# Kernel tuning notes

Measured on AMD Instinct MI355X. Metric: run time of the kernel, lower is better.

Reference implementation:

```python
import jax, jax.numpy as jnp
import numpy as np

N = 50000      # nodes
E = 400000     # edges per hop
IN = 256       # in_channels
H = 4          # heads
C = 64         # out_channels per head
NEG = 0.2      # leaky relu negative slope


def setup_inputs() -> dict:
    key = jax.random.key(0)
    ks = jax.random.split(key, 10)
    x = jax.random.normal(ks[0], (N, IN), dtype=jnp.float32)
    edge_index1 = jax.random.randint(ks[1], (2, E), 0, N, dtype=jnp.int32)
    edge_index2 = jax.random.randint(ks[2], (2, E), 0, N, dtype=jnp.int32)
    s = 0.05
    Wl0 = jax.random.normal(ks[3], (IN, H * C), dtype=jnp.float32) * s
    Wr0 = jax.random.normal(ks[4], (IN, H * C), dtype=jnp.float32) * s
    att0 = jax.random.normal(ks[5], (H, C), dtype=jnp.float32) * s
    Wl1 = jax.random.normal(ks[6], (IN, H * C), dtype=jnp.float32) * s
    Wr1 = jax.random.normal(ks[7], (IN, H * C), dtype=jnp.float32) * s
    att1 = jax.random.normal(ks[8], (H, C), dtype=jnp.float32) * s
    return {"x": x, "Wl0": Wl0, "Wr0": Wr0, "att0": att0,
            "Wl1": Wl1, "Wr1": Wr1, "att1": att1,
            "edge_index1": edge_index1, "edge_index2": edge_index2}


def _gatv2_hop(x, Wl, Wr, att, src, dst):
    """One GATv2Conv hop (bias=False, residual=False, eval-mode dropout, concat=False)."""
    n = x.shape[0]
    xl = (x @ Wl).reshape(n, H, C)   # source-side projection
    xr = (x @ Wr).reshape(n, H, C)   # target-side projection
    # edge-wise GATv2 score: a^T leaky_relu(x_l[j] + x_r[i])
    m = jax.nn.leaky_relu(xl[src] + xr[dst], NEG)            # [E, H, C]
    e = jnp.einsum('ehc,hc->eh', m, att)                     # [E, H]
    # segment softmax over incoming edges of each destination node
    e_max = jax.lax.stop_gradient(
        jax.ops.segment_max(e, dst, num_segments=n))         # [N, H]
    ex = jnp.exp(e - e_max[dst])
    denom = jax.ops.segment_sum(ex, dst, num_segments=n)     # [N, H]
    alpha = ex / (denom[dst] + 1e-16)                        # [E, H]
    msg = xl[src] * alpha[:, :, None]                        # [E, H, C]
    out = jax.ops.segment_sum(msg, dst, num_segments=n)      # [N, H, C]
    return out.mean(axis=1)                                  # concat=False -> mean heads


def reference(x, Wl0, Wr0, att0, Wl1, Wr1, att1, edge_index1, edge_index2):
    n = x.shape[0]
    # hop 0: add_self_loops=True
    loop = jnp.arange(n, dtype=edge_index1.dtype)
    src0 = jnp.concatenate([edge_index1[0], loop])
    dst0 = jnp.concatenate([edge_index1[1], loop])
    out = _gatv2_hop(x, Wl0, Wr0, att0, src0, dst0)
    # hop 1: no self loops, scaled by 1/(k+1) = 1/2
    out = out + _gatv2_hop(x, Wl1, Wr1, att1, edge_index2[0], edge_index2[1]) / 2.0
    return out
```

## Files before the change

### kernel.cpp

```cpp
#include <hip/hip_runtime.h>

typedef unsigned int uint;
typedef unsigned short ushort;

typedef __bf16 bf16x8 __attribute__((ext_vector_type(8)));
typedef float f32x4 __attribute__((ext_vector_type(4)));

#define CAP 48
#define RSTR 136

__device__ __forceinline__ float bf2f(ushort u) {
    return __uint_as_float(((uint)u) << 16);
}
__device__ __forceinline__ ushort f2bf(float f) {
    uint u = __float_as_uint(f);
    u += 0x7fffu + ((u >> 16) & 1u);
    return (ushort)(u >> 16);
}
__device__ __forceinline__ void load_lds16(const ushort* g, ushort* l) {
    __builtin_amdgcn_global_load_lds(
        (const __attribute__((address_space(1))) void*)g,
        (__attribute__((address_space(3))) void*)l, 16, 0, 0);
}

template<int CTRL>
__device__ __forceinline__ float dppadd(float p) {
    int t = __builtin_amdgcn_update_dpp(0, __float_as_int(p), CTRL, 0xf, 0xf, true);
    return p + __int_as_float(t);
}

__global__ __launch_bounds__(256) void prep(
    const float* __restrict__ X, ushort* __restrict__ Xb, int Nrows, int Mpad,
    const float* __restrict__ Wl0, const float* __restrict__ Wr0,
    const float* __restrict__ Wl1, const float* __restrict__ Wr1,
    ushort* __restrict__ Wt,
    int* __restrict__ cnt0, int* __restrict__ cnt1)
{
    const int BX = Mpad / 8;
    int blk = blockIdx.x;
    if (blk < BX) {
        int i = blk * 256 + threadIdx.x;
        int base = i * 8;
        int row = base >> 8;
        ushort o[8];
        if (row < Nrows) {
            float4 v0 = *(const float4*)(X + base);
            float4 v1 = *(const float4*)(X + base + 4);
            o[0] = f2bf(v0.x); o[1] = f2bf(v0.y); o[2] = f2bf(v0.z); o[3] = f2bf(v0.w);
            o[4] = f2bf(v1.x); o[5] = f2bf(v1.y); o[6] = f2bf(v1.z); o[7] = f2bf(v1.w);
        } else {
#pragma unroll
            for (int j = 0; j < 8; j++) o[j] = 0;
        }
        *(uint4*)(Xb + base) = *(const uint4*)o;
        return;
    }
    blk -= BX;
    if (blk < 1024) {
        int n = blk;
        int k = threadIdx.x;
        const float* W = (n < 256) ? Wl0 : (n < 512) ? Wr0 : (n < 768) ? Wl1 : Wr1;
        Wt[n * 256 + k] = f2bf(W[k * 256 + (n & 255)]);
        return;
    }
    blk -= 1024;
    int d = blk * 256 + threadIdx.x;
    if (d < Nrows) {
        cnt0[d] = 0;
        cnt1[d] = 0;
    }
}

__global__ __launch_bounds__(256) void csr_scatter2(
    const int* __restrict__ ei1, const int* __restrict__ ei2,
    int* __restrict__ cnt0, int* __restrict__ srcs0,
    int* __restrict__ cnt1, int* __restrict__ srcs1,
    int E1, int E2)
{
    int e = blockIdx.x * 256 + threadIdx.x;
    if (e < E1) {
        int d = ei1[E1 + e];
        int pos = atomicAdd(&cnt0[d], 1);
        if (pos < CAP) srcs0[(size_t)d * CAP + pos] = ei1[e];
    } else if (e < E1 + E2) {
        int e2 = e - E1;
        int d = ei2[E2 + e2];
        int pos = atomicAdd(&cnt1[d], 1);
        if (pos < CAP) srcs1[(size_t)d * CAP + pos] = ei2[e2];
    }
}

__global__ __launch_bounds__(256, 2) void gemm_mfma(
    const ushort* __restrict__ Xb,
    const ushort* __restrict__ Wt,
    ushort* __restrict__ XP,
    int Nrows)
{
    __shared__ ushort SH[2 * 128 * 64];
    ushort* As = SH;
    ushort* Bs = SH + 128 * 64;

    const int tid = threadIdx.x;
    const int w = tid >> 6, l = tid & 63;
    const int wm = w & 1, wn = w >> 1;
    const int m0 = blockIdx.y * 128;
    const int n0g = blockIdx.x * 128;

    f32x4 acc[4][4];
#pragma unroll
    for (int i = 0; i < 4; i++)
#pragma unroll
        for (int j = 0; j < 4; j++) acc[i][j] = (f32x4)(0.f);

    const int fr = l & 15, fq = l >> 4;
    int a_off[2][4], b_off[2][4];
#pragma unroll
    for (int g = 0; g < 2; g++)
#pragma unroll
        for (int t = 0; t < 4; t++) {
            int c = g * 4 + fq;
            int rA = wm * 64 + t * 16 + fr;
            a_off[g][t] = (rA * 8 + ((c + rA) & 7)) * 8;
            int rB = wn * 64 + t * 16 + fr;
            b_off[g][t] = (rB * 8 + ((c + rB) & 7)) * 8;
        }

    for (int k0 = 0; k0 < 256; k0 += 64) {
        __syncthreads();
#pragma unroll
        for (int rnd = 0; rnd < 4; rnd++) {
            int slot = rnd * 256 + tid;
            int row = slot >> 3;
            int c = ((slot & 7) - row) & 7;
            load_lds16(Xb + (size_t)(m0 + row) * 256 + k0 + c * 8,
                       &As[(rnd * 256 + w * 64) * 8]);
            load_lds16(Wt + (size_t)(n0g + row) * 256 + k0 + c * 8,
                       &Bs[(rnd * 256 + w * 64) * 8]);
        }
        __syncthreads();

#pragma unroll
        for (int g = 0; g < 2; g++) {
            bf16x8 a[4], b[4];
#pragma unroll
            for (int t = 0; t < 4; t++) {
                a[t] = *(const bf16x8*)(As + a_off[g][t]);
                b[t] = *(const bf16x8*)(Bs + b_off[g][t]);
            }
#pragma unroll
            for (int mi = 0; mi < 4; mi++)
#pragma unroll
                for (int ni = 0; ni < 4; ni++)
                    acc[mi][ni] = __builtin_amdgcn_mfma_f32_16x16x32_bf16(
                        a[mi], b[ni], acc[mi][ni], 0, 0, 0);
        }
    }

    ushort* OUT = XP + (size_t)(n0g >> 8) * ((size_t)Nrows * 256);
    const int colbase = n0g & 255;
    const int cb = wn * 64 + fr;
#pragma unroll
    for (int r = 0; r < 2; r++) {
        __syncthreads();
#pragma unroll
        for (int mm = 0; mm < 2; mm++) {
            int mi = 2 * r + mm;
            int brb = (wm * 32 + mm * 16 + fq * 4) * RSTR + cb;
#pragma unroll
            for (int reg = 0; reg < 4; reg++)
#pragma unroll
                for (int ni = 0; ni < 4; ni++)
                    SH[brb + reg * RSTR + ni * 16] = f2bf(acc[mi][ni][reg]);
        }
        __syncthreads();
        int br = tid >> 2;
        int grow = m0 + (br >> 5) * 64 + (2 * r + ((br >> 4) & 1)) * 16 + (br & 15);
        bool ok = (grow < Nrows);
        int cc = (tid & 3) * 8;
#pragma unroll
        for (int q = 0; q < 4; q++) {
            uint4 v = *(const uint4*)(SH + br * RSTR + cc + q * 32);
            if (ok) *(uint4*)(OUT + (size_t)grow * 256 + colbase + cc + q * 32) = v;
        }
    }
}

__device__ __forceinline__ uint4 pair_load(const ushort* __restrict__ XL, int sv,
                                           int e, int cp, uint hl, uint sub16)
{
    int eA = (e     < cp) ? e     : cp;
    int eB = (e + 1 < cp) ? e + 1 : cp;
    uint sA = (uint)__builtin_amdgcn_readlane(sv, eA) * 512u;
    uint sB = (uint)__builtin_amdgcn_readlane(sv, eB) * 512u;
    uint off = sA + hl * (sB - sA) + sub16;
    return *(const uint4*)((const char*)XL + off);
}

__device__ __forceinline__ void eaccp(uint4 raw, int deadB, uint hl,
    const float* __restrict__ xr8, const float* __restrict__ av,
    float* __restrict__ acc, float& den)
{
    float x[8];
    x[0] = __uint_as_float(raw.x << 16);
    x[1] = __uint_as_float(raw.x & 0xffff0000u);
    x[2] = __uint_as_float(raw.y << 16);
    x[3] = __uint_as_float(raw.y & 0xffff0000u);
    x[4] = __uint_as_float(raw.z << 16);
    x[5] = __uint_as_float(raw.z & 0xffff0000u);
    x[6] = __uint_as_float(raw.w << 16);
    x[7] = __uint_as_float(raw.w & 0xffff0000u);
    float p0 = 0.f, p1 = 0.f;
#pragma unroll
    for (int j = 0; j < 4; j++) {
        float t = x[j] + xr8[j];
        float lr = fmaxf(t, 0.2f * t);
        p0 = fmaf(av[j], lr, p0);
    }
#pragma unroll
    for (int j = 4; j < 8; j++) {
        float t = x[j] + xr8[j];
        float lr = fmaxf(t, 0.2f * t);
        p1 = fmaf(av[j], lr, p1);
    }
    float p = p0 + p1;
    p = dppadd<0xB1>(p);
    p = dppadd<0x4E>(p);
    p = dppadd<0x141>(p);
    float pe = __expf(p);
    if (deadB & (int)hl) pe = 0.f;
    den += pe;
#pragma unroll
    for (int j = 0; j < 8; j++) acc[j] = fmaf(pe, x[j], acc[j]);
}

__device__ __forceinline__ void gat_hop(
    const ushort* __restrict__ XL, const ushort* __restrict__ XR,
    const float* __restrict__ att, const int* __restrict__ cnt,
    const int* __restrict__ srcs, int self, int d, int lane,
    uint hl, uint sub, uint sub16,
    float* __restrict__ acc, float& den)
{
    uint4 xrr = *(const uint4*)((const char*)XR + (uint)d * 512u + sub16);
    float xr8[8];
    xr8[0] = __uint_as_float(xrr.x << 16);
    xr8[1] = __uint_as_float(xrr.x & 0xffff0000u);
    xr8[2] = __uint_as_float(xrr.y << 16);
    xr8[3] = __uint_as_float(xrr.y & 0xffff0000u);
    xr8[4] = __uint_as_float(xrr.z << 16);
    xr8[5] = __uint_as_float(xrr.z & 0xffff0000u);
    xr8[6] = __uint_as_float(xrr.w << 16);
    xr8[7] = __uint_as_float(xrr.w & 0xffff0000u);
    float av[8];
    *(float4*)(av)     = *(const float4*)(att + sub * 8);
    *(float4*)(av + 4) = *(const float4*)(att + sub * 8 + 4);

#pragma unroll
    for (int j = 0; j < 8; j++) acc[j] = 0.f;
    den = 0.f;

    int m = __builtin_amdgcn_readfirstlane(cnt[d]);
    if (m > CAP) m = CAP;
    const int mt = m + self;
    if (mt <= 0) return;

    int idx = lane - self;
    int mm1 = (m > 0) ? (m - 1) : 0;
    int slot = idx < 0 ? 0 : (idx > mm1 ? mm1 : idx);
    int sv = srcs[(size_t)d * CAP + slot];
    if (self && lane == 0) sv = d;

    const int cp = mt - 1;
    uint4 pf0 = pair_load(XL, sv, 0, cp, hl, sub16);
    uint4 pf1 = pair_load(XL, sv, 2, cp, hl, sub16);
    for (int i = 0; i < mt; i += 4) {
        uint4 c0 = pf0, c1 = pf1;
        pf0 = pair_load(XL, sv, i + 4, cp, hl, sub16);
        pf1 = pair_load(XL, sv, i + 6, cp, hl, sub16);
        eaccp(c0, (i + 1 >= mt) ? 1 : 0, hl, xr8, av, acc, den);
        if (i + 2 < mt)
            eaccp(c1, (i + 3 >= mt) ? 1 : 0, hl, xr8, av, acc, den);
    }
}

__global__ __launch_bounds__(256) void gat_fused(
    const ushort* __restrict__ XL0, const ushort* __restrict__ XR0,
    const float* __restrict__ att0,
    const int* __restrict__ cnt0, const int* __restrict__ srcs0,
    int self0, float scale0,
    const ushort* __restrict__ XL1, const ushort* __restrict__ XR1,
    const float* __restrict__ att1,
    const int* __restrict__ cnt1, const int* __restrict__ srcs1,
    float scale1,
    const float* __restrict__ base, float* __restrict__ outp, int N)
{
    int d = blockIdx.x * 4 + (threadIdx.x >> 6);
    if (d >= N) return;
    int lane = threadIdx.x & 63;
    uint hl = (uint)(lane >> 5);
    uint sub = (uint)(lane & 31);
    uint sub16 = sub * 16u;

    float acc0[8], den0;
    gat_hop(XL0, XR0, att0, cnt0, srcs0, self0, d, lane, hl, sub, sub16, acc0, den0);

    float v[8];
    den0 += __shfl_xor(den0, 32);
    float s0 = scale0 / (den0 + 1e-16f);
    if (cnt1) {
        float acc1[8], den1;
        gat_hop(XL1, XR1, att1, cnt1, srcs1, 0, d, lane, hl, sub, sub16, acc1, den1);
        den1 += __shfl_xor(den1, 32);
        float s1 = scale1 / (den1 + 1e-16f);
#pragma unroll
        for (int j = 0; j < 8; j++) v[j] = acc0[j] * s0 + acc1[j] * s1;
    } else {
#pragma unroll
        for (int j = 0; j < 8; j++) v[j] = acc0[j] * s0;
    }
#pragma unroll
    for (int j = 0; j < 8; j++) {
        v[j] += __shfl_xor(v[j], 8);
        v[j] += __shfl_xor(v[j], 16);
        v[j] += __shfl_xor(v[j], 32);
    }
    if (lane < 8) {
        float* dst = outp + (size_t)d * 64 + lane * 8;
        float4 w0 = {v[0], v[1], v[2], v[3]};
        float4 w1 = {v[4], v[5], v[6], v[7]};
        if (base) {
            float4 b0 = *(const float4*)(base + (size_t)d * 64 + lane * 8);
            float4 b1 = *(const float4*)(base + (size_t)d * 64 + lane * 8 + 4);
            w0.x += b0.x; w0.y += b0.y; w0.z += b0.z; w0.w += b0.w;
            w1.x += b1.x; w1.y += b1.y; w1.z += b1.z; w1.w += b1.w;
        }
        *(float4*)dst = w0;
        *(float4*)(dst + 4) = w1;
    }
}

extern "C" void kernel_launch(void* const* d_in, const int* in_sizes, int n_in,
                              void* d_out, int out_size, void* d_ws, size_t ws_size,
                              hipStream_t stream)
{
    const float* x    = (const float*)d_in[0];
    const float* Wl0  = (const float*)d_in[1];
    const float* Wr0  = (const float*)d_in[2];
    const float* att0 = (const float*)d_in[3];
    const float* Wl1  = (const float*)d_in[4];
    const float* Wr1  = (const float*)d_in[5];
    const float* att1 = (const float*)d_in[6];
    const int* ei1 = (const int*)d_in[7];
    const int* ei2 = (const int*)d_in[8];

    const int N  = in_sizes[0] / 256;
    const int E1 = in_sizes[7] / 2;
    const int E2 = in_sizes[8] / 2;
    const int Mpad = ((N + 127) / 128) * 128;
    const size_t NB = (size_t)N * 256;

    char* ws = (char*)d_ws;
    size_t off = 0;
    ushort* Xb  = (ushort*)(ws + off); off += (size_t)Mpad * 256 * sizeof(ushort);
    ushort* Wt  = (ushort*)(ws + off); off += (size_t)1024 * 256 * sizeof(ushort);
    int* cnt0   = (int*)(ws + off);    off += (size_t)N * sizeof(int);
    int* cnt1   = (int*)(ws + off);    off += (size_t)N * sizeof(int);
    int* srcs0  = (int*)(ws + off);    off += (size_t)N * CAP * sizeof(int);
    int* srcs1  = (int*)(ws + off);    off += (size_t)N * CAP * sizeof(int);
    ushort* XP  = (ushort*)(ws + off);
    size_t need_mega = off + 4 * NB * sizeof(ushort);
    const bool mega = (ws_size >= need_mega);
    float* outf = (float*)d_out;

    const int BX = Mpad / 8;
    int prep_blocks = BX + 1024 + (N + 255) / 256;
    prep<<<prep_blocks, 256, 0, stream>>>(x, Xb, N, Mpad, Wl0, Wr0, Wl1, Wr1,
                                          Wt, cnt0, cnt1);
    const int SB = (E1 + E2 + 255) / 256;
    csr_scatter2<<<SB, 256, 0, stream>>>(
        ei1, ei2, cnt0, srcs0, cnt1, srcs1, E1, E2);

    int aggblk = (N + 3) / 4;
    if (mega) {
        gemm_mfma<<<dim3(8, Mpad / 128), 256, 0, stream>>>(Xb, Wt, XP, N);
        gat_fused<<<aggblk, 256, 0, stream>>>(
            XP, XP + NB, att0, cnt0, srcs0, 1, 0.25f,
            XP + 2 * NB, XP + 3 * NB, att1, cnt1, srcs1, 0.125f,
            nullptr, outf, N);
    } else {
        gemm_mfma<<<dim3(4, Mpad / 128), 256, 0, stream>>>(Xb, Wt, XP, N);
        gat_fused<<<aggblk, 256, 0, stream>>>(
            XP, XP + NB, att0, cnt0, srcs0, 1, 0.25f,
            nullptr, nullptr, nullptr, nullptr, nullptr, 0.f,
            nullptr, outf, N);
        gemm_mfma<<<dim3(4, Mpad / 128), 256, 0, stream>>>(Xb, Wt + 512 * 256, XP, N);
        gat_fused<<<aggblk, 256, 0, stream>>>(
            XP, XP + NB, att1, cnt1, srcs1, 0, 0.125f,
            nullptr, nullptr, nullptr, nullptr, nullptr, 0.f,
            outf, outf, N);
    }
}
```

Baseline: 270.9 us.

## Merge CSR scatter into GEMM launch and pack aggregation math as float2

The edge scatter kernel is folded into the GEMM launch as extra blocks in a 1D grid, so the atomic CSR build runs alongside the MFMA tiles instead of as its own serialized launch. Counter zeroing moves from the prep kernel to a hipMemsetAsync. The edge accumulation math is rewritten on float2 vectors so the compiler can emit packed FP32 ops (v_pk_fma/v_pk_mul) on MI355X. This removes one launch and idle time between kernels, but the GEMM blocks, which use 2-per-CU occupancy, now share the machine with atomic-heavy scatter blocks.

```diff
diff --git a/kernel.cpp b/kernel.cpp
--- a/kernel.cpp
+++ b/kernel.cpp
@@ -5,6 +5,7 @@
 
 typedef __bf16 bf16x8 __attribute__((ext_vector_type(8)));
 typedef float f32x4 __attribute__((ext_vector_type(4)));
+typedef float f32x2 __attribute__((ext_vector_type(2)));
 
 #define CAP 48
 #define RSTR 136
@@ -22,6 +23,12 @@
         (const __attribute__((address_space(1))) void*)g,
         (__attribute__((address_space(3))) void*)l, 16, 0, 0);
 }
+__device__ __forceinline__ f32x2 up2(uint u) {
+    f32x2 r;
+    r.x = __uint_as_float(u << 16);
+    r.y = __uint_as_float(u & 0xffff0000u);
+    return r;
+}
 
 template<int CTRL>
 __device__ __forceinline__ float dppadd(float p) {
@@ -33,8 +40,7 @@
     const float* __restrict__ X, ushort* __restrict__ Xb, int Nrows, int Mpad,
     const float* __restrict__ Wl0, const float* __restrict__ Wr0,
     const float* __restrict__ Wl1, const float* __restrict__ Wr1,
-    ushort* __restrict__ Wt,
-    int* __restrict__ cnt0, int* __restrict__ cnt1)
+    ushort* __restrict__ Wt)
 {
     const int BX = Mpad / 8;
     int blk = blockIdx.x;
@@ -56,46 +62,38 @@
         return;
     }
     blk -= BX;
-    if (blk < 1024) {
-        int n = blk;
-        int k = threadIdx.x;
-        const float* W = (n < 256) ? Wl0 : (n < 512) ? Wr0 : (n < 768) ? Wl1 : Wr1;
-        Wt[n * 256 + k] = f2bf(W[k * 256 + (n & 255)]);
-        return;
-    }
-    blk -= 1024;
-    int d = blk * 256 + threadIdx.x;
-    if (d < Nrows) {
-        cnt0[d] = 0;
-        cnt1[d] = 0;
-    }
-}
-
-__global__ __launch_bounds__(256) void csr_scatter2(
+    int n = blk;
+    int k = threadIdx.x;
+    const float* W = (n < 256) ? Wl0 : (n < 512) ? Wr0 : (n < 768) ? Wl1 : Wr1;
+    Wt[n * 256 + k] = f2bf(W[k * 256 + (n & 255)]);
+}
+
+__global__ __launch_bounds__(256, 2) void gemm_scatter(
+    const ushort* __restrict__ Xb,
+    const ushort* __restrict__ Wt,
+    ushort* __restrict__ XP,
+    int Nrows, int GB, int cshift,
     const int* __restrict__ ei1, const int* __restrict__ ei2,
     int* __restrict__ cnt0, int* __restrict__ srcs0,
     int* __restrict__ cnt1, int* __restrict__ srcs1,
     int E1, int E2)
 {
-    int e = blockIdx.x * 256 + threadIdx.x;
-    if (e < E1) {
-        int d = ei1[E1 + e];
-        int pos = atomicAdd(&cnt0[d], 1);
-        if (pos < CAP) srcs0[(size_t)d * CAP + pos] = ei1[e];
-    } else if (e < E1 + E2) {
-        int e2 = e - E1;
-        int d = ei2[E2 + e2];
-        int pos = atomicAdd(&cnt1[d], 1);
-        if (pos < CAP) srcs1[(size_t)d * CAP + pos] = ei2[e2];
-    }
-}
-
-__global__ __launch_bounds__(256, 2) void gemm_mfma(
-    const ushort* __restrict__ Xb,
-    const ushort* __restrict__ Wt,
-    ushort* __restrict__ XP,
-    int Nrows)
-{
+    int blk = blockIdx.x;
+    if (blk >= GB) {
+        int e = (blk - GB) * 256 + threadIdx.x;
+        if (e < E1) {
+            int d = ei1[E1 + e];
+            int pos = atomicAdd(&cnt0[d], 1);
+            if (pos < CAP) srcs0[(size_t)d * CAP + pos] = ei1[e];
+        } else if (e < E1 + E2) {
+            int e2 = e - E1;
+            int d = ei2[E2 + e2];
+            int pos = atomicAdd(&cnt1[d], 1);
+            if (pos < CAP) srcs1[(size_t)d * CAP + pos] = ei2[e2];
+        }
+        return;
+    }
+
     __shared__ ushort SH[2 * 128 * 64];
     ushort* As = SH;
     ushort* Bs = SH + 128 * 64;
@@ -103,8 +101,8 @@
     const int tid = threadIdx.x;
     const int w = tid >> 6, l = tid & 63;
     const int wm = w & 1, wn = w >> 1;
-    const int m0 = blockIdx.y * 128;
-    const int n0g = blockIdx.x * 128;
+    const int m0 = (blk >> cshift) * 128;
+    const int n0g = (blk & ((1 << cshift) - 1)) * 128;
 
     f32x4 acc[4][4];
 #pragma unroll
@@ -197,32 +195,24 @@
 }
 
 __device__ __forceinline__ void eaccp(uint4 raw, int deadB, uint hl,
-    const float* __restrict__ xr8, const float* __restrict__ av,
-    float* __restrict__ acc, float& den)
-{
-    float x[8];
-    x[0] = __uint_as_float(raw.x << 16);
-    x[1] = __uint_as_float(raw.x & 0xffff0000u);
-    x[2] = __uint_as_float(raw.y << 16);
-    x[3] = __uint_as_float(raw.y & 0xffff0000u);
-    x[4] = __uint_as_float(raw.z << 16);
-    x[5] = __uint_as_float(raw.z & 0xffff0000u);
-    x[6] = __uint_as_float(raw.w << 16);
-    x[7] = __uint_as_float(raw.w & 0xffff0000u);
-    float p0 = 0.f, p1 = 0.f;
-#pragma unroll
-    for (int j = 0; j < 4; j++) {
-        float t = x[j] + xr8[j];
-        float lr = fmaxf(t, 0.2f * t);
-        p0 = fmaf(av[j], lr, p0);
-    }
-#pragma unroll
-    for (int j = 4; j < 8; j++) {
-        float t = x[j] + xr8[j];
-        float lr = fmaxf(t, 0.2f * t);
-        p1 = fmaf(av[j], lr, p1);
-    }
-    float p = p0 + p1;
+    const f32x2* __restrict__ xr2, const f32x2* __restrict__ av2,
+    f32x2* __restrict__ acc, float& den)
+{
+    f32x2 xv[4];
+    xv[0] = up2(raw.x);
+    xv[1] = up2(raw.y);
+    xv[2] = up2(raw.z);
+    xv[3] = up2(raw.w);
+    f32x2 p2 = (f32x2)(0.f);
+#pragma unroll
+    for (int k = 0; k < 4; k++) {
+        f32x2 t = xv[k] + xr2[k];
+        f32x2 u = t * 0.2f;
+        t.x = fmaxf(t.x, u.x);
+        t.y = fmaxf(t.y, u.y);
+        p2 += t * av2[k];
+    }
+    float p = p2.x + p2.y;
     p = dppadd<0xB1>(p);
     p = dppadd<0x4E>(p);
     p = dppadd<0x141>(p);
@@ -230,7 +220,7 @@
     if (deadB & (int)hl) pe = 0.f;
     den += pe;
 #pragma unroll
-    for (int j = 0; j < 8; j++) acc[j] = fmaf(pe, x[j], acc[j]);
+    for (int k = 0; k < 4; k++) acc[k] += xv[k] * pe;
 }
 
 __device__ __forceinline__ void gat_hop(
@@ -238,24 +228,24 @@
     const float* __restrict__ att, const int* __restrict__ cnt,
     const int* __restrict__ srcs, int self, int d, int lane,
     uint hl, uint sub, uint sub16,
-    float* __restrict__ acc, float& den)
+    f32x2* __restrict__ acc, float& den)
 {
     uint4 xrr = *(const uint4*)((const char*)XR + (uint)d * 512u + sub16);
-    float xr8[8];
-    xr8[0] = __uint_as_float(xrr.x << 16);
-    xr8[1] = __uint_as_float(xrr.x & 0xffff0000u);
-    xr8[2] = __uint_as_float(xrr.y << 16);
-    xr8[3] = __uint_as_float(xrr.y & 0xffff0000u);
-    xr8[4] = __uint_as_float(xrr.z << 16);
-    xr8[5] = __uint_as_float(xrr.z & 0xffff0000u);
-    xr8[6] = __uint_as_float(xrr.w << 16);
-    xr8[7] = __uint_as_float(xrr.w & 0xffff0000u);
-    float av[8];
-    *(float4*)(av)     = *(const float4*)(att + sub * 8);
-    *(float4*)(av + 4) = *(const float4*)(att + sub * 8 + 4);
-
-#pragma unroll
-    for (int j = 0; j < 8; j++) acc[j] = 0.f;
+    f32x2 xr2[4];
+    xr2[0] = up2(xrr.x);
+    xr2[1] = up2(xrr.y);
+    xr2[2] = up2(xrr.z);
+    xr2[3] = up2(xrr.w);
+    float4 a0 = *(const float4*)(att + sub * 8);
+    float4 a1 = *(const float4*)(att + sub * 8 + 4);
+    f32x2 av2[4];
+    av2[0].x = a0.x; av2[0].y = a0.y;
+    av2[1].x = a0.z; av2[1].y = a0.w;
+    av2[2].x = a1.x; av2[2].y = a1.y;
+    av2[3].x = a1.z; av2[3].y = a1.w;
+
+#pragma unroll
+    for (int k = 0; k < 4; k++) acc[k] = (f32x2)(0.f);
     den = 0.f;
 
     int m = __builtin_amdgcn_readfirstlane(cnt[d]);
@@ -276,9 +266,9 @@
         uint4 c0 = pf0, c1 = pf1;
         pf0 = pair_load(XL, sv, i + 4, cp, hl, sub16);
         pf1 = pair_load(XL, sv, i + 6, cp, hl, sub16);
-        eaccp(c0, (i + 1 >= mt) ? 1 : 0, hl, xr8, av, acc, den);
+        eaccp(c0, (i + 1 >= mt) ? 1 : 0, hl, xr2, av2, acc, den);
         if (i + 2 < mt)
-            eaccp(c1, (i + 3 >= mt) ? 1 : 0, hl, xr8, av, acc, den);
+            eaccp(c1, (i + 3 >= mt) ? 1 : 0, hl, xr2, av2, acc, den);
     }
 }
 
@@ -300,22 +290,30 @@
     uint sub = (uint)(lane & 31);
     uint sub16 = sub * 16u;
 
-    float acc0[8], den0;
+    f32x2 acc0[4];
+    float den0;
     gat_hop(XL0, XR0, att0, cnt0, srcs0, self0, d, lane, hl, sub, sub16, acc0, den0);
 
     float v[8];
     den0 += __shfl_xor(den0, 32);
     float s0 = scale0 / (den0 + 1e-16f);
     if (cnt1) {
-        float acc1[8], den1;
+        f32x2 acc1[4];
+        float den1;
         gat_hop(XL1, XR1, att1, cnt1, srcs1, 0, d, lane, hl, sub, sub16, acc1, den1);
         den1 += __shfl_xor(den1, 32);
         float s1 = scale1 / (den1 + 1e-16f);
 #pragma unroll
-        for (int j = 0; j < 8; j++) v[j] = acc0[j] * s0 + acc1[j] * s1;
+        for (int k = 0; k < 4; k++) {
+            v[2 * k]     = acc0[k].x * s0 + acc1[k].x * s1;
+            v[2 * k + 1] = acc0[k].y * s0 + acc1[k].y * s1;
+        }
     } else {
 #pragma unroll
-        for (int j = 0; j < 8; j++) v[j] = acc0[j] * s0;
+        for (int k = 0; k < 4; k++) {
+            v[2 * k]     = acc0[k].x * s0;
+            v[2 * k + 1] = acc0[k].y * s0;
+        }
     }
 #pragma unroll
     for (int j = 0; j < 8; j++) {
@@ -371,28 +369,34 @@
     const bool mega = (ws_size >= need_mega);
     float* outf = (float*)d_out;
 
+    hipMemsetAsync(cnt0, 0, 2 * (size_t)N * sizeof(int), stream);
+
     const int BX = Mpad / 8;
-    int prep_blocks = BX + 1024 + (N + 255) / 256;
-    prep<<<prep_blocks, 256, 0, stream>>>(x, Xb, N, Mpad, Wl0, Wr0, Wl1, Wr1,
-                                          Wt, cnt0, cnt1);
+    prep<<<BX + 1024, 256, 0, stream>>>(x, Xb, N, Mpad, Wl0, Wr0, Wl1, Wr1, Wt);
+
     const int SB = (E1 + E2 + 255) / 256;
-    csr_scatter2<<<SB, 256, 0, stream>>>(
-        ei1, ei2, cnt0, srcs0, cnt1, srcs1, E1, E2);
-
     int aggblk = (N + 3) / 4;
     if (mega) {
-        gemm_mfma<<<dim3(8, Mpad / 128), 256, 0, stream>>>(Xb, Wt, XP, N);
+        int GB = 8 * (Mpad / 128);
+        gemm_scatter<<<GB + SB, 256, 0, stream>>>(
+            Xb, Wt, XP, N, GB, 3,
+            ei1, ei2, cnt0, srcs0, cnt1, srcs1, E1, E2);
         gat_fused<<<aggblk, 256, 0, stream>>>(
             XP, XP + NB, att0, cnt0, srcs0, 1, 0.25f,
             XP + 2 * NB, XP + 3 * NB, att1, cnt1, srcs1, 0.125f,
             nullptr, outf, N);
     } else {
-        gemm_mfma<<<dim3(4, Mpad / 128), 256, 0, stream>>>(Xb, Wt, XP, N);
+        int GB = 4 * (Mpad / 128);
+        gemm_scatter<<<GB + SB, 256, 0, stream>>>(
+            Xb, Wt, XP, N, GB, 2,
+            ei1, ei2, cnt0, srcs0, cnt1, srcs1, E1, E2);
         gat_fused<<<aggblk, 256, 0, stream>>>(
             XP, XP + NB, att0, cnt0, srcs0, 1, 0.25f,
             nullptr, nullptr, nullptr, nullptr, nullptr, 0.f,
             nullptr, outf, N);
-        gemm_mfma<<<dim3(4, Mpad / 128), 256, 0, stream>>>(Xb, Wt + 512 * 256, XP, N);
+        gemm_scatter<<<GB, 256, 0, stream>>>(
+            Xb, Wt + 512 * 256, XP, N, GB, 2,
+            nullptr, nullptr, cnt0, srcs0, cnt1, srcs1, 0, 0);
         gat_fused<<<aggblk, 256, 0, stream>>>(
             XP, XP + NB, att1, cnt1, srcs1, 0, 0.125f,
             nullptr, nullptr, nullptr, nullptr, nullptr, 0.f,
```

After: 280.5 us. 1.04x slower.
